# Kernel tuning notes

Hardware: AMD Instinct MI355X
Metric: run time of the kernel (lower is better)

Reference implementation:

```python
import jax, jax.numpy as jnp
import numpy as np

B, M, A = 16384, 1024, 512
SETTLING_STEPS = 10
TAU = 0.1


def setup_inputs() -> dict:
    key = jax.random.key(0)
    k0, k1, k2 = jax.random.split(key, 3)
    x = jax.random.normal(k0, (B, M), dtype=jnp.float32)
    # input_proj: Linear(micro_dim, attractor_dim) -> weight (A, M), bias (A)
    W_in = jax.random.normal(k1, (A, M), dtype=jnp.float32) * (1.0 / np.sqrt(M))
    b_in = jnp.zeros((A,), dtype=jnp.float32)
    # J: orthogonal-init * 0.9 in original; here a scaled random matrix keeps
    # spectral radius moderate so tanh does not fully saturate (same math).
    J = jax.random.normal(k2, (A, A), dtype=jnp.float32) * (0.09 / np.sqrt(A))
    return {"x": x, "W_in": W_in, "b_in": b_in, "J": J}


def reference(x, W_in, b_in, J):
    tau = max(TAU, 1e-6)
    # drive = input_proj(x), computed once outside the settling loop
    drive = x @ W_in.T + b_in  # [B, A]
    sigma0 = jnp.zeros((x.shape[0], J.shape[0]), dtype=x.dtype)

    def step(sigma, _):
        # recurrent = F.linear(sigma, J) / tau; sigma = tanh(drive + recurrent)
        sigma = jnp.tanh(drive + (sigma @ J.T) * (1.0 / tau))
        return sigma, None

    sigma, _ = jax.lax.scan(step, sigma0, None, length=SETTLING_STEPS)
    return sigma
```

## Files before the change

kernel.cpp:

```cpp
#include <hip/hip_runtime.h>
#include <stdint.h>


#define B_DIM 16384
#define M_DIM 1024
#define A_DIM 512

typedef short bf16x8 __attribute__((ext_vector_type(8)));
typedef float f32x4 __attribute__((ext_vector_type(4)));

#define GLDS16(g, l)                                                        \
  __builtin_amdgcn_global_load_lds(                                         \
      (const __attribute__((address_space(1))) unsigned int*)(g),           \
      (__attribute__((address_space(3))) unsigned int*)(l), 16, 0, 0)

__device__ __forceinline__ unsigned short f2bf(float f) {
  unsigned int u = __float_as_uint(f);
  unsigned int r = (u + 0x7FFFu + ((u >> 16) & 1u)) >> 16;
  return (unsigned short)r;
}
__device__ __forceinline__ float bf2f(unsigned short s) {
  return __uint_as_float(((unsigned int)s) << 16);
}
__device__ __forceinline__ float fast_tanh(float x) {
  float t = __expf(2.0f * x);
  return fmaf(-2.0f, __builtin_amdgcn_rcpf(t + 1.0f), 1.0f);
}

__global__ void split_kernel(const float* __restrict__ src,
                             unsigned short* __restrict__ hi,
                             unsigned short* __restrict__ lo,
                             int n, float scale) {
  int i = blockIdx.x * 256 + threadIdx.x;
  if (i < n) {
    float v = src[i] * scale;
    unsigned short h = f2bf(v);
    hi[i] = h;
    lo[i] = f2bf(v - bf2f(h));
  }
}

__global__ __launch_bounds__(256) void drive_kernel(
    const float* __restrict__ x, const unsigned short* __restrict__ Whi,
    const unsigned short* __restrict__ Wlo, const float* __restrict__ bias,
    float* __restrict__ drive, unsigned short* __restrict__ sig) {
  __shared__ __align__(16) unsigned short Ah[128][40];
  __shared__ __align__(16) unsigned short Al[128][40];
  __shared__ __align__(16) unsigned short Bh[128][40];
  __shared__ __align__(16) unsigned short Bl[128][40];

  const int t = threadIdx.x;
  const int bm = blockIdx.y, bn = blockIdx.x;
  const int row = t >> 1, half = t & 1;
  const int lane = t & 63, wave = t >> 6;
  const int wm = wave >> 1, wn = wave & 1;
  const int quad = lane >> 4, l16 = lane & 15;

  f32x4 acc[4][4] = {};

  const float* xp = x + (size_t)(bm * 128 + row) * M_DIM + half * 16;
  const unsigned short* wh = Whi + (size_t)(bn * 128 + row) * M_DIM + half * 16;
  const unsigned short* wl = Wlo + (size_t)(bn * 128 + row) * M_DIM + half * 16;

  for (int k0 = 0; k0 < M_DIM; k0 += 32) {
    float4 v[4];
#pragma unroll
    for (int q = 0; q < 4; ++q) v[q] = *(const float4*)(xp + k0 + 4 * q);
    unsigned short hiv[16], lov[16];
#pragma unroll
    for (int q = 0; q < 4; ++q) {
      float fv[4] = {v[q].x, v[q].y, v[q].z, v[q].w};
#pragma unroll
      for (int e = 0; e < 4; ++e) {
        unsigned short h = f2bf(fv[e]);
        hiv[4 * q + e] = h;
        lov[4 * q + e] = f2bf(fv[e] - bf2f(h));
      }
    }
    *(uint4*)&Ah[row][half * 16]     = *(uint4*)&hiv[0];
    *(uint4*)&Ah[row][half * 16 + 8] = *(uint4*)&hiv[8];
    *(uint4*)&Al[row][half * 16]     = *(uint4*)&lov[0];
    *(uint4*)&Al[row][half * 16 + 8] = *(uint4*)&lov[8];
    *(uint4*)&Bh[row][half * 16]     = *(const uint4*)(wh + k0);
    *(uint4*)&Bh[row][half * 16 + 8] = *(const uint4*)(wh + k0 + 8);
    *(uint4*)&Bl[row][half * 16]     = *(const uint4*)(wl + k0);
    *(uint4*)&Bl[row][half * 16 + 8] = *(const uint4*)(wl + k0 + 8);
    __syncthreads();

    bf16x8 ah[4], al[4], bh[4], bl[4];
#pragma unroll
    for (int i = 0; i < 4; ++i) {
      ah[i] = *(const bf16x8*)&Ah[wm * 64 + i * 16 + l16][quad * 8];
      al[i] = *(const bf16x8*)&Al[wm * 64 + i * 16 + l16][quad * 8];
    }
#pragma unroll
    for (int j = 0; j < 4; ++j) {
      bh[j] = *(const bf16x8*)&Bh[wn * 64 + j * 16 + l16][quad * 8];
      bl[j] = *(const bf16x8*)&Bl[wn * 64 + j * 16 + l16][quad * 8];
    }
#pragma unroll
    for (int i = 0; i < 4; ++i)
#pragma unroll
      for (int j = 0; j < 4; ++j) {
        acc[i][j] = __builtin_amdgcn_mfma_f32_16x16x32_bf16(ah[i], bh[j], acc[i][j], 0, 0, 0);
        acc[i][j] = __builtin_amdgcn_mfma_f32_16x16x32_bf16(ah[i], bl[j], acc[i][j], 0, 0, 0);
        acc[i][j] = __builtin_amdgcn_mfma_f32_16x16x32_bf16(al[i], bh[j], acc[i][j], 0, 0, 0);
      }
    __syncthreads();
  }

#pragma unroll
  for (int i = 0; i < 4; ++i)
#pragma unroll
    for (int j = 0; j < 4; ++j) {
      int gcol = bn * 128 + wn * 64 + j * 16 + l16;
      float bv = bias[gcol];
#pragma unroll
      for (int r = 0; r < 4; ++r) {
        int grow = bm * 128 + wm * 64 + i * 16 + quad * 4 + r;
        float dv = acc[i][j][r] + bv;
        size_t idx = (size_t)grow * A_DIM + gcol;
        drive[idx] = dv;
        sig[idx] = f2bf(fast_tanh(dv));
      }
    }
}

__global__ __launch_bounds__(256) void step_kernel(
    const unsigned short* __restrict__ sin_, const unsigned short* __restrict__ Jhi,
    const unsigned short* __restrict__ Jlo, const float* __restrict__ drive,
    unsigned short* __restrict__ sout, float* __restrict__ outf, int last) {
  __shared__ __align__(16) unsigned short As[128 * 64];
  __shared__ __align__(16) unsigned short Bhs[128 * 64];
  __shared__ __align__(16) unsigned short Bls[128 * 64];

  const int t = threadIdx.x;
  const int bm = blockIdx.y, bn = blockIdx.x;
  const int lane = t & 63, wave = t >> 6;
  const int wm = wave >> 1, wn = wave & 1;
  const int quad = lane >> 4, l16 = lane & 15;
  const int rl = lane >> 3;
  const int gsrc = (lane & 7) ^ rl;

  f32x4 acc[4][4] = {};

  const unsigned short* aT = sin_ + (size_t)(bm * 128) * A_DIM;
  const unsigned short* bhT = Jhi + (size_t)(bn * 128) * A_DIM;
  const unsigned short* blT = Jlo + (size_t)(bn * 128) * A_DIM;

  for (int k0 = 0; k0 < A_DIM; k0 += 64) {
#pragma unroll
    for (int q = 0; q < 4; ++q) {
      const int c = wave * 4 + q;
      const size_t goff = (size_t)(c * 8 + rl) * A_DIM + k0 + gsrc * 8;
      GLDS16(aT + goff, &As[c * 512]);
      GLDS16(bhT + goff, &Bhs[c * 512]);
      GLDS16(blT + goff, &Bls[c * 512]);
    }
    __syncthreads();

#pragma unroll
    for (int h = 0; h < 2; ++h) {
      bf16x8 af[4], bhf[4], blf[4];
#pragma unroll
      for (int i = 0; i < 4; ++i) {
        const int r = wm * 64 + i * 16 + l16;
        af[i] = *(const bf16x8*)&As[r * 64 + 8 * ((4 * h + quad) ^ (r & 7))];
      }
#pragma unroll
      for (int j = 0; j < 4; ++j) {
        const int r = wn * 64 + j * 16 + l16;
        const int off = r * 64 + 8 * ((4 * h + quad) ^ (r & 7));
        bhf[j] = *(const bf16x8*)&Bhs[off];
        blf[j] = *(const bf16x8*)&Bls[off];
      }
#pragma unroll
      for (int i = 0; i < 4; ++i)
#pragma unroll
        for (int j = 0; j < 4; ++j) {
          acc[i][j] = __builtin_amdgcn_mfma_f32_16x16x32_bf16(af[i], bhf[j], acc[i][j], 0, 0, 0);
          acc[i][j] = __builtin_amdgcn_mfma_f32_16x16x32_bf16(af[i], blf[j], acc[i][j], 0, 0, 0);
        }
    }
    __syncthreads();
  }

#pragma unroll
  for (int i = 0; i < 4; ++i)
#pragma unroll
    for (int j = 0; j < 4; ++j) {
      int gcol = bn * 128 + wn * 64 + j * 16 + l16;
#pragma unroll
      for (int r = 0; r < 4; ++r) {
        int grow = bm * 128 + wm * 64 + i * 16 + quad * 4 + r;
        size_t idx = (size_t)grow * A_DIM + gcol;
        float v = fast_tanh(drive[idx] + acc[i][j][r]);
        if (last) outf[idx] = v;
        else sout[idx] = f2bf(v);
      }
    }
}

extern "C" void kernel_launch(void* const* d_in, const int* in_sizes, int n_in,
                              void* d_out, int out_size, void* d_ws, size_t ws_size,
                              hipStream_t stream) {
  const float* x = (const float*)d_in[0];
  const float* W = (const float*)d_in[1];
  const float* b = (const float*)d_in[2];
  const float* J = (const float*)d_in[3];
  float* out = (float*)d_out;

  char* ws = (char*)d_ws;
  float* drive         = (float*)(ws);
  unsigned short* sigA = (unsigned short*)(ws + 33554432);
  unsigned short* sigB = (unsigned short*)(ws + 50331648);
  unsigned short* Whi  = (unsigned short*)(ws + 67108864);
  unsigned short* Wlo  = (unsigned short*)(ws + 68157440);
  unsigned short* Jhi  = (unsigned short*)(ws + 69206016);
  unsigned short* Jlo  = (unsigned short*)(ws + 69730304);

  const int nW = A_DIM * M_DIM;
  const int nJ = A_DIM * A_DIM;
  split_kernel<<<(nW + 255) / 256, 256, 0, stream>>>(W, Whi, Wlo, nW, 1.0f);
  split_kernel<<<(nJ + 255) / 256, 256, 0, stream>>>(J, Jhi, Jlo, nJ, 10.0f);

  dim3 grid(A_DIM / 128, B_DIM / 128);
  drive_kernel<<<grid, 256, 0, stream>>>(x, Whi, Wlo, b, drive, sigA);

  unsigned short* cur = sigA;
  unsigned short* nxt = sigB;
  for (int s = 0; s < 9; ++s) {
    step_kernel<<<grid, 256, 0, stream>>>(cur, Jhi, Jlo, drive, nxt, out, s == 8);
    unsigned short* tmp = cur; cur = nxt; nxt = tmp;
  }
}
```

Before: 514.2 us.

## Fuse all settling steps into one persistent kernel keeping sigma in LDS

Replaces the nine separate step kernel launches with a single settle kernel. Each 512-thread block owns 64 batch rows for every column, keeps that tile's drive values in registers and the bf16 sigma tile in shared memory, and iterates all steps internally. The J hi/lo fragments are read straight from global memory (L2) on each step. This removes the per-step global round trips of sigma and drive and the launch gaps, at the cost of 64KB of LDS per block, heavy register use, fewer blocks (256), and J re-reads with no LDS staging.

New measurement: 967.3 us. 88.1% more time.

```diff
diff --git a/kernel.cpp b/kernel.cpp
--- a/kernel.cpp
+++ b/kernel.cpp
@@ -8,11 +8,6 @@
 
 typedef short bf16x8 __attribute__((ext_vector_type(8)));
 typedef float f32x4 __attribute__((ext_vector_type(4)));
-
-#define GLDS16(g, l)                                                        \
-  __builtin_amdgcn_global_load_lds(                                         \
-      (const __attribute__((address_space(1))) unsigned int*)(g),           \
-      (__attribute__((address_space(3))) unsigned int*)(l), 16, 0, 0)
 
 __device__ __forceinline__ unsigned short f2bf(float f) {
   unsigned int u = __float_as_uint(f);
@@ -43,7 +38,7 @@
 __global__ __launch_bounds__(256) void drive_kernel(
     const float* __restrict__ x, const unsigned short* __restrict__ Whi,
     const unsigned short* __restrict__ Wlo, const float* __restrict__ bias,
-    float* __restrict__ drive, unsigned short* __restrict__ sig) {
+    float* __restrict__ drive) {
   __shared__ __align__(16) unsigned short Ah[128][40];
   __shared__ __align__(16) unsigned short Al[128][40];
   __shared__ __align__(16) unsigned short Bh[128][40];
@@ -118,87 +113,130 @@
 #pragma unroll
       for (int r = 0; r < 4; ++r) {
         int grow = bm * 128 + wm * 64 + i * 16 + quad * 4 + r;
-        float dv = acc[i][j][r] + bv;
-        size_t idx = (size_t)grow * A_DIM + gcol;
-        drive[idx] = dv;
-        sig[idx] = f2bf(fast_tanh(dv));
-      }
-    }
-}
-
-__global__ __launch_bounds__(256) void step_kernel(
-    const unsigned short* __restrict__ sin_, const unsigned short* __restrict__ Jhi,
-    const unsigned short* __restrict__ Jlo, const float* __restrict__ drive,
-    unsigned short* __restrict__ sout, float* __restrict__ outf, int last) {
-  __shared__ __align__(16) unsigned short As[128 * 64];
-  __shared__ __align__(16) unsigned short Bhs[128 * 64];
-  __shared__ __align__(16) unsigned short Bls[128 * 64];
+        drive[(size_t)grow * A_DIM + gcol] = acc[i][j][r] + bv;
+      }
+    }
+}
+
+__global__ __launch_bounds__(512) void settle_kernel(
+    const unsigned short* __restrict__ Jhi,
+    const unsigned short* __restrict__ Jlo,
+    const float* __restrict__ drive, float* __restrict__ outf) {
+  __shared__ __align__(16) unsigned short smem[64 * 512];
 
   const int t = threadIdx.x;
-  const int bm = blockIdx.y, bn = blockIdx.x;
-  const int lane = t & 63, wave = t >> 6;
-  const int wm = wave >> 1, wn = wave & 1;
+  const int lane = t & 63, w = t >> 6;
   const int quad = lane >> 4, l16 = lane & 15;
-  const int rl = lane >> 3;
-  const int gsrc = (lane & 7) ^ rl;
-
-  f32x4 acc[4][4] = {};
-
-  const unsigned short* aT = sin_ + (size_t)(bm * 128) * A_DIM;
-  const unsigned short* bhT = Jhi + (size_t)(bn * 128) * A_DIM;
-  const unsigned short* blT = Jlo + (size_t)(bn * 128) * A_DIM;
-
-  for (int k0 = 0; k0 < A_DIM; k0 += 64) {
-#pragma unroll
-    for (int q = 0; q < 4; ++q) {
-      const int c = wave * 4 + q;
-      const size_t goff = (size_t)(c * 8 + rl) * A_DIM + k0 + gsrc * 8;
-      GLDS16(aT + goff, &As[c * 512]);
-      GLDS16(bhT + goff, &Bhs[c * 512]);
-      GLDS16(blT + goff, &Bls[c * 512]);
-    }
-    __syncthreads();
-
-#pragma unroll
-    for (int h = 0; h < 2; ++h) {
-      bf16x8 af[4], bhf[4], blf[4];
+  const int r0 = blockIdx.x * 64;
+
+  float dreg[4][4][4];
+#pragma unroll
+  for (int i = 0; i < 4; ++i)
+#pragma unroll
+    for (int j = 0; j < 4; ++j) {
+      const float* dp =
+          drive + (size_t)(r0 + i * 16 + quad * 4) * A_DIM + w * 64 + j * 16 + l16;
+#pragma unroll
+      for (int rr = 0; rr < 4; ++rr) dreg[i][j][rr] = dp[(size_t)rr * A_DIM];
+    }
+
+#pragma unroll
+  for (int i = 0; i < 4; ++i)
+#pragma unroll
+    for (int rr = 0; rr < 4; ++rr) {
+      const int r = i * 16 + quad * 4 + rr;
+#pragma unroll
+      for (int j = 0; j < 4; ++j) {
+        const int c = w * 64 + j * 16 + l16;
+        smem[r * 512 + (((c >> 3) ^ (r & 7)) << 3) + (c & 7)] =
+            f2bf(fast_tanh(dreg[i][j][rr]));
+      }
+    }
+
+  const unsigned short* jph[4];
+  const unsigned short* jpl[4];
+#pragma unroll
+  for (int j = 0; j < 4; ++j) {
+    const size_t ro = (size_t)(w * 64 + j * 16 + l16) * A_DIM + quad * 8;
+    jph[j] = Jhi + ro;
+    jpl[j] = Jlo + ro;
+  }
+  int abase[4][2];
+#pragma unroll
+  for (int i = 0; i < 4; ++i) {
+    const int r = i * 16 + l16;
+#pragma unroll
+    for (int h = 0; h < 2; ++h)
+      abase[i][h] = r * 512 + (((h * 4 + quad) ^ (r & 7)) << 3);
+  }
+
+  __syncthreads();
+
+  for (int s = 0; s < 9; ++s) {
+    f32x4 acc[4][4] = {};
+    for (int kb = 0; kb < 8; ++kb) {
+      const int k0 = kb * 64;
+      bf16x8 a0[4], a1[4], bh0[4], bh1[4];
+#pragma unroll
+      for (int j = 0; j < 4; ++j) {
+        bh0[j] = *(const bf16x8*)(jph[j] + k0);
+        bh1[j] = *(const bf16x8*)(jph[j] + k0 + 32);
+      }
 #pragma unroll
       for (int i = 0; i < 4; ++i) {
-        const int r = wm * 64 + i * 16 + l16;
-        af[i] = *(const bf16x8*)&As[r * 64 + 8 * ((4 * h + quad) ^ (r & 7))];
-      }
-#pragma unroll
-      for (int j = 0; j < 4; ++j) {
-        const int r = wn * 64 + j * 16 + l16;
-        const int off = r * 64 + 8 * ((4 * h + quad) ^ (r & 7));
-        bhf[j] = *(const bf16x8*)&Bhs[off];
-        blf[j] = *(const bf16x8*)&Bls[off];
+        a0[i] = *(const bf16x8*)&smem[abase[i][0] + kb * 64];
+        a1[i] = *(const bf16x8*)&smem[abase[i][1] + kb * 64];
       }
 #pragma unroll
       for (int i = 0; i < 4; ++i)
 #pragma unroll
         for (int j = 0; j < 4; ++j) {
-          acc[i][j] = __builtin_amdgcn_mfma_f32_16x16x32_bf16(af[i], bhf[j], acc[i][j], 0, 0, 0);
-          acc[i][j] = __builtin_amdgcn_mfma_f32_16x16x32_bf16(af[i], blf[j], acc[i][j], 0, 0, 0);
-        }
-    }
-    __syncthreads();
-  }
-
-#pragma unroll
-  for (int i = 0; i < 4; ++i)
-#pragma unroll
-    for (int j = 0; j < 4; ++j) {
-      int gcol = bn * 128 + wn * 64 + j * 16 + l16;
-#pragma unroll
-      for (int r = 0; r < 4; ++r) {
-        int grow = bm * 128 + wm * 64 + i * 16 + quad * 4 + r;
-        size_t idx = (size_t)grow * A_DIM + gcol;
-        float v = fast_tanh(drive[idx] + acc[i][j][r]);
-        if (last) outf[idx] = v;
-        else sout[idx] = f2bf(v);
-      }
-    }
+          acc[i][j] = __builtin_amdgcn_mfma_f32_16x16x32_bf16(a0[i], bh0[j], acc[i][j], 0, 0, 0);
+          acc[i][j] = __builtin_amdgcn_mfma_f32_16x16x32_bf16(a1[i], bh1[j], acc[i][j], 0, 0, 0);
+        }
+      bf16x8 bl0[4], bl1[4];
+#pragma unroll
+      for (int j = 0; j < 4; ++j) {
+        bl0[j] = *(const bf16x8*)(jpl[j] + k0);
+        bl1[j] = *(const bf16x8*)(jpl[j] + k0 + 32);
+      }
+#pragma unroll
+      for (int i = 0; i < 4; ++i)
+#pragma unroll
+        for (int j = 0; j < 4; ++j) {
+          acc[i][j] = __builtin_amdgcn_mfma_f32_16x16x32_bf16(a0[i], bl0[j], acc[i][j], 0, 0, 0);
+          acc[i][j] = __builtin_amdgcn_mfma_f32_16x16x32_bf16(a1[i], bl1[j], acc[i][j], 0, 0, 0);
+        }
+    }
+
+    if (s == 8) {
+#pragma unroll
+      for (int i = 0; i < 4; ++i)
+#pragma unroll
+        for (int j = 0; j < 4; ++j) {
+          float* op =
+              outf + (size_t)(r0 + i * 16 + quad * 4) * A_DIM + w * 64 + j * 16 + l16;
+#pragma unroll
+          for (int rr = 0; rr < 4; ++rr)
+            op[(size_t)rr * A_DIM] = fast_tanh(dreg[i][j][rr] + acc[i][j][rr]);
+        }
+    } else {
+      __syncthreads();
+#pragma unroll
+      for (int i = 0; i < 4; ++i)
+#pragma unroll
+        for (int rr = 0; rr < 4; ++rr) {
+          const int r = i * 16 + quad * 4 + rr;
+#pragma unroll
+          for (int j = 0; j < 4; ++j) {
+            const int c = w * 64 + j * 16 + l16;
+            smem[r * 512 + (((c >> 3) ^ (r & 7)) << 3) + (c & 7)] =
+                f2bf(fast_tanh(dreg[i][j][rr] + acc[i][j][rr]));
+          }
+        }
+      __syncthreads();
+    }
+  }
 }
 
 extern "C" void kernel_launch(void* const* d_in, const int* in_sizes, int n_in,
@@ -211,26 +249,19 @@
   float* out = (float*)d_out;
 
   char* ws = (char*)d_ws;
-  float* drive         = (float*)(ws);
-  unsigned short* sigA = (unsigned short*)(ws + 33554432);
-  unsigned short* sigB = (unsigned short*)(ws + 50331648);
-  unsigned short* Whi  = (unsigned short*)(ws + 67108864);
-  unsigned short* Wlo  = (unsigned short*)(ws + 68157440);
-  unsigned short* Jhi  = (unsigned short*)(ws + 69206016);
-  unsigned short* Jlo  = (unsigned short*)(ws + 69730304);
+  float* drive        = (float*)(ws);
+  unsigned short* Whi = (unsigned short*)(ws + 33554432);
+  unsigned short* Wlo = (unsigned short*)(ws + 34603008);
+  unsigned short* Jhi = (unsigned short*)(ws + 35651584);
+  unsigned short* Jlo = (unsigned short*)(ws + 36175872);
 
   const int nW = A_DIM * M_DIM;
   const int nJ = A_DIM * A_DIM;
   split_kernel<<<(nW + 255) / 256, 256, 0, stream>>>(W, Whi, Wlo, nW, 1.0f);
   split_kernel<<<(nJ + 255) / 256, 256, 0, stream>>>(J, Jhi, Jlo, nJ, 10.0f);
 
-  dim3 grid(A_DIM / 128, B_DIM / 128);
-  drive_kernel<<<grid, 256, 0, stream>>>(x, Whi, Wlo, b, drive, sigA);
-
-  unsigned short* cur = sigA;
-  unsigned short* nxt = sigB;
-  for (int s = 0; s < 9; ++s) {
-    step_kernel<<<grid, 256, 0, stream>>>(cur, Jhi, Jlo, drive, nxt, out, s == 8);
-    unsigned short* tmp = cur; cur = nxt; nxt = tmp;
-  }
-}
+  dim3 dgrid(A_DIM / 128, B_DIM / 128);
+  drive_kernel<<<dgrid, 256, 0, stream>>>(x, Whi, Wlo, b, drive);
+
+  settle_kernel<<<B_DIM / 64, 512, 0, stream>>>(Jhi, Jlo, drive, out);
+}
```
